# Performance work log

Measured on AMD Instinct MI355X. Metric: run time of the kernel, lower is better.

Reference implementation:

```python
import jax, jax.numpy as jnp
import numpy as np

T, B, D_IN, E, HA, HB, D_OUT = 64, 64, 4096, 128, 128, 128, 4096


def setup_inputs() -> dict:
    key = jax.random.key(0)
    ks = jax.random.split(key, 18)

    def u(k, shape, fan):
        b = 1.0 / np.sqrt(fan)
        return jax.random.uniform(k, shape, jnp.float32, -b, b)

    return {
        "x": jax.random.uniform(ks[0], (T, B, D_IN), jnp.float32),
        "W_emb": u(ks[1], (E, D_IN), D_IN), "b_emb": u(ks[2], (E,), D_IN),
        "W_ih_a": u(ks[3], (3 * HA, E), HA), "W_hh_a": u(ks[4], (3 * HA, HA), HA),
        "b_ih_a": u(ks[5], (3 * HA,), HA), "b_hh_a": u(ks[6], (3 * HA,), HA),
        "W_ih_b": u(ks[7], (3 * HB, E), HB), "W_hh_b": u(ks[8], (3 * HB, HB), HB),
        "b_ih_b": u(ks[9], (3 * HB,), HB), "b_hh_b": u(ks[10], (3 * HB,), HB),
        "w_alpha": u(ks[11], (1, HA), HA), "b_alpha": u(ks[12], (1,), HA),
        "W_beta": u(ks[13], (E, HB), HB), "b_beta": u(ks[14], (E,), HB),
        "W_out": u(ks[15], (D_OUT, E), E), "b_out": u(ks[16], (D_OUT,), E),
    }


def _gru_states(emb, W_ih, W_hh, b_ih, b_hh):
    # For every query position i, run a GRU over the reversed prefix
    # emb[i], emb[i-1], ..., emb[0] from h0 = 0. All T queries are batched.
    # Returns hs[s, i, b, h] = hidden of query i after step s (input emb[i-s]).
    Tlen, Bsz, _ = emb.shape
    H = W_hh.shape[1]
    i_arr = jnp.arange(Tlen)

    def step(h, s):
        idx = jnp.clip(i_arr - s, 0, Tlen - 1)          # (T,) input index per query
        xs = emb[idx]                                    # (T, B, E)
        gi = xs @ W_ih.T + b_ih                          # (T, B, 3H)
        gh = h @ W_hh.T + b_hh
        i_r, i_z, i_n = jnp.split(gi, 3, axis=-1)
        h_r, h_z, h_n = jnp.split(gh, 3, axis=-1)
        r = jax.nn.sigmoid(i_r + h_r)
        z = jax.nn.sigmoid(i_z + h_z)
        n = jnp.tanh(i_n + r * h_n)
        h_new = (1.0 - z) * n + z * h
        return h_new, h_new

    h0 = jnp.zeros((Tlen, Bsz, H), emb.dtype)
    _, hs = jax.lax.scan(step, h0, jnp.arange(Tlen))
    return hs  # (S, T, B, H)


def _retain_forward(x, W_emb, b_emb, W_ih_a, W_hh_a, b_ih_a, b_hh_a,
                    W_ih_b, W_hh_b, b_ih_b, b_hh_b, w_alpha, b_alpha,
                    W_beta, b_beta, W_out, b_out):
    Tlen = x.shape[0]
    emb = x @ W_emb.T + b_emb                            # (T, B, E)

    hs_a = _gru_states(emb, W_ih_a, W_hh_a, b_ih_a, b_hh_a)  # (S, T, B, HA)
    hs_b = _gru_states(emb, W_ih_b, W_hh_b, b_ih_b, b_hh_b)  # (S, T, B, HB)

    i_arr = jnp.arange(Tlen)
    # reverse_h[i, j] = hidden after processing emb[i..j] (reverse order) = hs[i - j, i]
    rev = jnp.clip(i_arr[:, None] - i_arr[None, :], 0, Tlen - 1)  # (T, T)
    rh_a = hs_a[rev, i_arr[:, None]] * 0.5               # (T, T, B, HA)
    rh_b = hs_b[rev, i_arr[:, None]] * 0.5               # (T, T, B, HB)

    mask = (i_arr[None, :] <= i_arr[:, None])            # (T, T): j <= i valid
    logits = jnp.einsum('ijbh,h->ijb', rh_a, w_alpha[0]) + b_alpha[0]
    logits = jnp.where(mask[:, :, None], logits, -1e9)
    alpha = jax.nn.softmax(logits, axis=1)               # softmax over prefix steps j
    alpha = alpha * mask[:, :, None].astype(alpha.dtype)

    beta = jnp.tanh(rh_b @ W_beta.T + b_beta)            # (T, T, B, E)

    # c[i] = mean_{j<=i} alpha[i,j] * beta[i,j] * emb[j]
    c = jnp.einsum('ijb,ijbe->ibe', alpha, beta * emb[None, :, :, :])
    counts = jnp.arange(1, Tlen + 1, dtype=c.dtype)[:, None, None]
    c = c / counts

    return jax.nn.sigmoid(c @ W_out.T + b_out)           # (T, B, D_OUT)


def reference(x, W_emb, b_emb, W_ih_a, W_hh_a, b_ih_a, b_hh_a,
              W_ih_b, W_hh_b, b_ih_b, b_hh_b, w_alpha, b_alpha,
              W_beta, b_beta, W_out, b_out):
    return _retain_forward(x, W_emb, b_emb, W_ih_a, W_hh_a, b_ih_a, b_hh_a,
                           W_ih_b, W_hh_b, b_ih_b, b_hh_b, w_alpha, b_alpha,
                           W_beta, b_beta, W_out, b_out)
```

## Files before the change

kernel.cpp:

```cpp
#include <hip/hip_runtime.h>
#include <hip/hip_bf16.h>


typedef __attribute__((ext_vector_type(8))) short short8;
typedef __attribute__((ext_vector_type(4))) float f32x4;
typedef _Float16 half8 __attribute__((ext_vector_type(8)));

#define MFMA16(a, b, c) __builtin_amdgcn_mfma_f32_16x16x32_bf16((a), (b), (c), 0, 0, 0)

#define LOG2E 1.4426950408889634f
#define TLOG2E 2.8853900817779268f

__device__ __forceinline__ unsigned short f2bf(float f) {
  unsigned int u = __float_as_uint(f);
  u += 0x7fffu + ((u >> 16) & 1u);
  return (unsigned short)(u >> 16);
}
__device__ __forceinline__ unsigned pkbf(float a, float b) {
  __hip_bfloat162 t = __float22bfloat162_rn(float2{a, b});
  return *reinterpret_cast<unsigned*>(&t);
}
__device__ __forceinline__ float ex2(float x) { return __builtin_amdgcn_exp2f(x); }
__device__ __forceinline__ float rcpa(float x) { return __builtin_amdgcn_rcpf(x); }
__device__ __forceinline__ float sigm2(float y) { return rcpa(1.0f + ex2(-y)); }
__device__ __forceinline__ float tanh2(float y) {
  float e = ex2(-fmaxf(y, -126.0f));
  return (1.0f - e) * rcpa(1.0f + e);
}

#define OFF_PART   0u
#define OFF_GI3    16777216u
#define OFF_EMBBF  25165824u
#define OFF_CBF    26214400u
#define OFF_WEMB   27262976u
#define OFF_WOUT   28311552u
#define OFF_WHHA   29360128u
#define OFF_WHHB   29458432u
#define OFF_WIH    29556736u
#define OFF_WBETA  29753344u

__global__ void k_prep(const float* W_emb, const float* W_out,
                       const float* W_hh_a, const float* W_hh_b,
                       const float* W_ih_a, const float* W_ih_b,
                       const float* W_beta,
                       unsigned* wemb, unsigned* wout,
                       unsigned* whha, unsigned* whhb,
                       unsigned* wih, unsigned* wbeta) {
  const unsigned total = 630784u;
  for (unsigned idx = blockIdx.x * 256u + threadIdx.x; idx < total;
       idx += gridDim.x * 256u) {
    unsigned i = idx;
    if (i < 262144u) { float2 v = ((const float2*)W_emb)[i]; wemb[i] = pkbf(v.x, v.y); continue; }
    i -= 262144u;
    if (i < 262144u) { float2 v = ((const float2*)W_out)[i]; wout[i] = pkbf(v.x, v.y); continue; }
    i -= 262144u;
    if (i < 24576u) {
      float2 v = ((const float2*)W_hh_a)[i];
      const float sc = ((i >> 13) == 2u) ? TLOG2E : LOG2E;
      whha[i] = pkbf(sc * v.x, sc * v.y); continue;
    }
    i -= 24576u;
    if (i < 24576u) {
      float2 v = ((const float2*)W_hh_b)[i];
      const float sc = ((i >> 13) == 2u) ? TLOG2E : LOG2E;
      whhb[i] = pkbf(sc * v.x, sc * v.y); continue;
    }
    i -= 24576u;
    if (i < 24576u) {
      float2 v = ((const float2*)W_ih_a)[i];
      const float sc = ((i >> 13) == 2u) ? TLOG2E : LOG2E;
      wih[i] = pkbf(sc * v.x, sc * v.y); continue;
    }
    i -= 24576u;
    if (i < 24576u) {
      float2 v = ((const float2*)W_ih_b)[i];
      const float sc = ((i >> 13) == 2u) ? TLOG2E : LOG2E;
      wih[24576u + i] = pkbf(sc * v.x, sc * v.y); continue;
    }
    i -= 24576u;
    { float2 v = ((const float2*)W_beta)[i]; wbeta[i] = pkbf(LOG2E * v.x, LOG2E * v.y); }
  }
}

__global__ __launch_bounds__(256) void k_emb_gemm(const float* __restrict__ x,
                                                  const unsigned short* __restrict__ wemb,
                                                  float* __restrict__ part) {
  const int mt = blockIdx.x >> 3, kc = blockIdx.x & 7;
  const int w = threadIdx.x >> 6, lane = threadIdx.x & 63, q = lane >> 4, ln = lane & 15;
  const f32x4 zero = {0.f, 0.f, 0.f, 0.f};
  f32x4 acc[2][8];
#pragma unroll
  for (int a = 0; a < 2; ++a)
#pragma unroll
    for (int b = 0; b < 8; ++b) acc[a][b] = zero;

  const float* xA = x + (size_t)(mt * 128 + (2 * w) * 16 + ln) * 4096 + kc * 512 + q * 8;
  const float* xB = xA + (size_t)16 * 4096;

  for (int kk = 0; kk < 16; ++kk) {
    const int ko = kk * 32;
    float4 u0 = *(const float4*)(xA + ko);
    float4 u1 = *(const float4*)(xA + ko + 4);
    float4 v0 = *(const float4*)(xB + ko);
    float4 v1 = *(const float4*)(xB + ko + 4);
    union { short8 v; unsigned u[4]; } a0, a1;
    a0.u[0] = pkbf(u0.x, u0.y); a0.u[1] = pkbf(u0.z, u0.w);
    a0.u[2] = pkbf(u1.x, u1.y); a0.u[3] = pkbf(u1.z, u1.w);
    a1.u[0] = pkbf(v0.x, v0.y); a1.u[1] = pkbf(v0.z, v0.w);
    a1.u[2] = pkbf(v1.x, v1.y); a1.u[3] = pkbf(v1.z, v1.w);
#pragma unroll
    for (int nt = 0; nt < 8; ++nt) {
      short8 b = *(const short8*)(wemb + (size_t)(nt * 16 + ln) * 4096 + kc * 512 + ko + q * 8);
      acc[0][nt] = MFMA16(a0.v, b, acc[0][nt]);
      acc[1][nt] = MFMA16(a1.v, b, acc[1][nt]);
    }
  }
#pragma unroll
  for (int st = 0; st < 2; ++st) {
    const int mbase = mt * 128 + (2 * w + st) * 16 + q * 4;
#pragma unroll
    for (int nt = 0; nt < 8; ++nt)
#pragma unroll
      for (int r = 0; r < 4; ++r)
        part[(size_t)kc * 524288 + (size_t)(mbase + r) * 128 + nt * 16 + ln] = acc[st][nt][r];
  }
}

__global__ void k_emb_reduce(const float* __restrict__ part, const float* __restrict__ b_emb,
                             _Float16* __restrict__ gih, unsigned* __restrict__ embbf) {
  const unsigned pidx = blockIdx.x * 256u + threadIdx.x;
  const unsigned e0 = (pidx * 2u) & 127u;
  const unsigned m = pidx >> 6;
  float2 s = ((const float2*)b_emb)[e0 >> 1];
#pragma unroll
  for (int kc = 0; kc < 8; ++kc) {
    float2 v = ((const float2*)(part + (size_t)kc * 524288u))[pidx];
    s.x += v.x; s.y += v.y;
  }
  gih[(size_t)m * 1024u + e0 * 8u + 6u] = (_Float16)s.x;
  gih[(size_t)m * 1024u + (e0 + 1u) * 8u + 6u] = (_Float16)s.y;
  embbf[pidx] = pkbf(s.x, s.y);
}

__global__ __launch_bounds__(256) void k_gi_gemm(const unsigned short* __restrict__ embbf,
                                                 const unsigned short* __restrict__ wih,
                                                 const float* __restrict__ b_ih_a,
                                                 const float* __restrict__ b_ih_b,
                                                 const float* __restrict__ b_hh_a,
                                                 const float* __restrict__ b_hh_b,
                                                 _Float16* __restrict__ gih) {
  const int mt = blockIdx.x / 6, nt6 = blockIdx.x % 6, nbase = nt6 * 128;
  const int w = threadIdx.x >> 6, lane = threadIdx.x & 63, q = lane >> 4, ln = lane & 15;
  const f32x4 zero = {0.f, 0.f, 0.f, 0.f};
  f32x4 acc[2][8];
#pragma unroll
  for (int a = 0; a < 2; ++a)
#pragma unroll
    for (int b = 0; b < 8; ++b) acc[a][b] = zero;

#pragma unroll
  for (int kk = 0; kk < 4; ++kk) {
    const int ko = kk * 32 + q * 8;
    short8 a0 = *(const short8*)(embbf + (size_t)(mt * 128 + (2 * w) * 16 + ln) * 128 + ko);
    short8 a1 = *(const short8*)(embbf + (size_t)(mt * 128 + (2 * w + 1) * 16 + ln) * 128 + ko);
#pragma unroll
    for (int nt = 0; nt < 8; ++nt) {
      short8 b = *(const short8*)(wih + (size_t)(nbase + nt * 16 + ln) * 128 + ko);
      acc[0][nt] = MFMA16(a0, b, acc[0][nt]);
      acc[1][nt] = MFMA16(a1, b, acc[1][nt]);
    }
  }
#pragma unroll
  for (int nt = 0; nt < 8; ++nt) {
    const int g = nbase + nt * 16 + ln;
    const int gg = g >> 7, kout = g & 127;
    float bias;
    if (g < 384) bias = b_ih_a[g] + ((gg < 2) ? b_hh_a[g] : 0.0f);
    else {
      const int g2 = g - 384;
      bias = b_ih_b[g2] + ((gg < 5) ? b_hh_b[g2] : 0.0f);
    }
    bias *= (gg == 2 || gg == 5) ? TLOG2E : LOG2E;
#pragma unroll
    for (int st = 0; st < 2; ++st) {
      const int mbase = mt * 128 + (2 * w + st) * 16 + q * 4;
#pragma unroll
      for (int r = 0; r < 4; ++r)
        gih[(size_t)(mbase + r) * 1024 + kout * 8 + gg] = (_Float16)(acc[st][nt][r] + bias);
    }
  }
}

__global__ __launch_bounds__(512) __attribute__((amdgpu_waves_per_eu(2, 2)))
void k_recur(const _Float16* __restrict__ gih,
             const unsigned short* __restrict__ whha, const unsigned short* __restrict__ whhb,
             const unsigned short* __restrict__ wbeta,
             const float* __restrict__ b_hh_a, const float* __restrict__ b_hh_b,
             const float* __restrict__ b_beta, const float* __restrict__ b_alpha,
             const float* __restrict__ w_alpha,
             unsigned short* __restrict__ cbf) {
  const int tid = threadIdx.x, w = tid >> 6, lane = tid & 63, q = lane >> 4, ln = lane & 15;
  const int p = blockIdx.x >> 3, btile = blockIdx.x & 7;
  const int i1 = p, i2 = 63 - p;
  const int kout = w * 16 + ln;

  __shared__ unsigned short hA[2][16 * 136], hB[2][16 * 136];

  for (int idx = tid; idx < 16 * 136; idx += 512) { hA[0][idx] = 0; hB[0][idx] = 0; }

  const int iq = (q < 2) ? i1 : i2;
  const _Float16* gp[4];
#pragma unroll
  for (int r = 0; r < 4; ++r) {
    const int b = btile * 8 + (q & 1) * 4 + r;
    gp[r] = gih + (size_t)(iq * 64 + b) * 1024 + kout * 8;
  }

  short8 fra[3][4], frb[3][4];
#pragma unroll
  for (int g = 0; g < 3; ++g) {
    const unsigned short* ba = whha + (size_t)(g * 128 + kout) * 128;
    const unsigned short* bb = whhb + (size_t)(g * 128 + kout) * 128;
#pragma unroll
    for (int kc = 0; kc < 4; ++kc) {
      fra[g][kc] = *(const short8*)(ba + kc * 32 + q * 8);
      frb[g][kc] = *(const short8*)(bb + kc * 32 + q * 8);
    }
  }
#pragma unroll
  for (int g = 0; g < 3; ++g)
#pragma unroll
    for (int kc = 0; kc < 4; ++kc) {
      asm volatile("" : "+a"(fra[g][kc]));
      asm volatile("" : "+a"(frb[g][kc]));
    }

  short8 fbe[4];
#pragma unroll
  for (int kc = 0; kc < 4; ++kc) {
    fbe[kc] = *(const short8*)(wbeta + (size_t)(w * 16 + ln) * 128 + kc * 32 + q * 8);
    asm volatile("" : "+a"(fbe[kc]));
  }

  short8 fal[4];
#pragma unroll
  for (int kc = 0; kc < 4; ++kc) {
    float4 w0 = *(const float4*)(w_alpha + kc * 32 + q * 8);
    float4 w1 = *(const float4*)(w_alpha + kc * 32 + q * 8 + 4);
    union { short8 v; unsigned u[4]; } t;
    t.u[0] = pkbf(0.5f * LOG2E * w0.x, 0.5f * LOG2E * w0.y);
    t.u[1] = pkbf(0.5f * LOG2E * w0.z, 0.5f * LOG2E * w0.w);
    t.u[2] = pkbf(0.5f * LOG2E * w1.x, 0.5f * LOG2E * w1.y);
    t.u[3] = pkbf(0.5f * LOG2E * w1.z, 0.5f * LOG2E * w1.w);
    const short8 z8 = {0, 0, 0, 0, 0, 0, 0, 0};
    fal[kc] = (ln == 0) ? t.v : z8;
    asm volatile("" : "+a"(fal[kc]));
  }

  const float bhnA = TLOG2E * b_hh_a[256 + kout];
  const float bhnB = TLOG2E * b_hh_b[256 + kout];
  const float bbet = TLOG2E * b_beta[kout];
  const float bal = LOG2E * b_alpha[0];

  float hRA[4], hRB[4], cac[4], lreg[4], embp[4];
#pragma unroll
  for (int r = 0; r < 4; ++r) { hRA[r] = 0.f; hRB[r] = 0.f; cac[r] = 0.f; lreg[r] = 0.f; embp[r] = 0.f; }

  const f32x4 zero = {0.f, 0.f, 0.f, 0.f};
  int jj = iq;
  half8 ngv[4];
#pragma unroll
  for (int r = 0; r < 4; ++r) ngv[r] = *(const half8*)gp[r];

  __syncthreads();

  for (int s = 0; s <= i2; ++s) {
    const int rb = s & 1, wb = rb ^ 1;

    half8 gv[4];
#pragma unroll
    for (int r = 0; r < 4; ++r) gv[r] = ngv[r];

    short8 haf[4], hbf[4];
#pragma unroll
    for (int kc = 0; kc < 4; ++kc) {
      haf[kc] = *(const short8*)(hA[rb] + ln * 136 + kc * 32 + q * 8);
      hbf[kc] = *(const short8*)(hB[rb] + ln * 136 + kc * 32 + q * 8);
    }

    f32x4 accA[3] = {zero, zero, zero}, accB[3] = {zero, zero, zero};
    f32x4 accV = zero, accL = zero;
#pragma unroll
    for (int kc = 0; kc < 4; ++kc) {
#pragma unroll
      for (int g = 0; g < 3; ++g) {
        accA[g] = MFMA16(haf[kc], fra[g][kc], accA[g]);
        accB[g] = MFMA16(hbf[kc], frb[g][kc], accB[g]);
      }
      accV = MFMA16(hbf[kc], fbe[kc], accV);
      accL = MFMA16(haf[kc], fal[kc], accL);
    }

    const bool act = ((unsigned)(s - 1) <= (unsigned)iq);
#pragma unroll
    for (int r = 0; r < 4; ++r) {
      const float logit =
          __int_as_float(__builtin_amdgcn_ds_swizzle(__float_as_int(accL[r]), 16)) + bal;
      const float pp = act ? ex2(logit) : 0.0f;
      lreg[r] += pp;
      const float beta = tanh2(accV[r] + bbet);
      cac[r] += pp * beta * embp[r];
    }

#pragma unroll
    for (int r = 0; r < 4; ++r) {
      const int rowoff = (q * 4 + r) * 136 + kout;
      const float rrA = sigm2((float)gv[r][0] + accA[0][r]);
      const float zzA = sigm2((float)gv[r][1] + accA[1][r]);
      const float nnA = tanh2((float)gv[r][2] + rrA * (accA[2][r] + bhnA));
      const float hnA = fmaf(zzA, hRA[r] - nnA, nnA);
      hRA[r] = hnA;
      hA[wb][rowoff] = f2bf(hnA);

      const float rrB = sigm2((float)gv[r][3] + accB[0][r]);
      const float zzB = sigm2((float)gv[r][4] + accB[1][r]);
      const float nnB = tanh2((float)gv[r][5] + rrB * (accB[2][r] + bhnB));
      const float hnB = fmaf(zzB, hRB[r] - nnB, nnB);
      hRB[r] = hnB;
      hB[wb][rowoff] = f2bf(hnB);

      embp[r] = (float)gv[r][6];
    }

    if (jj > 0) {
      --jj;
#pragma unroll
      for (int r = 0; r < 4; ++r) gp[r] -= 65536;
    }
#pragma unroll
    for (int r = 0; r < 4; ++r) ngv[r] = *(const half8*)gp[r];

    asm volatile("s_waitcnt lgkmcnt(0)\n\ts_barrier" ::: "memory");
  }

  {
    const int rb2 = (i2 + 1) & 1;
    short8 haf[4], hbf[4];
#pragma unroll
    for (int kc = 0; kc < 4; ++kc) {
      haf[kc] = *(const short8*)(hA[rb2] + ln * 136 + kc * 32 + q * 8);
      hbf[kc] = *(const short8*)(hB[rb2] + ln * 136 + kc * 32 + q * 8);
    }
    f32x4 accV = zero, accL = zero;
#pragma unroll
    for (int kc = 0; kc < 4; ++kc) {
      accV = MFMA16(hbf[kc], fbe[kc], accV);
      accL = MFMA16(haf[kc], fal[kc], accL);
    }
    const bool act = (iq == i2);
#pragma unroll
    for (int r = 0; r < 4; ++r) {
      const float logit =
          __int_as_float(__builtin_amdgcn_ds_swizzle(__float_as_int(accL[r]), 16)) + bal;
      const float pp = act ? ex2(logit) : 0.0f;
      lreg[r] += pp;
      const float beta = tanh2(accV[r] + bbet);
      cac[r] += pp * beta * embp[r];
    }
  }

#pragma unroll
  for (int r = 0; r < 4; ++r) {
    const int b = btile * 8 + (q & 1) * 4 + r;
    const float val = cac[r] * rcpa(lreg[r] * (float)(iq + 1));
    cbf[(size_t)(iq * 64 + b) * 128 + kout] = f2bf(val);
  }
}

__global__ __launch_bounds__(256) void k_out_gemm(const unsigned short* __restrict__ cbf,
                                                  const unsigned short* __restrict__ wout,
                                                  const float* __restrict__ b_out,
                                                  float* __restrict__ out) {
  const int mt = blockIdx.x >> 5, nt32 = blockIdx.x & 31, nbase = nt32 * 128;
  const int w = threadIdx.x >> 6, lane = threadIdx.x & 63, q = lane >> 4, ln = lane & 15;
  const f32x4 zero = {0.f, 0.f, 0.f, 0.f};
  f32x4 acc[2][8];
#pragma unroll
  for (int a = 0; a < 2; ++a)
#pragma unroll
    for (int b = 0; b < 8; ++b) acc[a][b] = zero;

#pragma unroll
  for (int kk = 0; kk < 4; ++kk) {
    const int ko = kk * 32 + q * 8;
    short8 a0 = *(const short8*)(cbf + (size_t)(mt * 128 + (2 * w) * 16 + ln) * 128 + ko);
    short8 a1 = *(const short8*)(cbf + (size_t)(mt * 128 + (2 * w + 1) * 16 + ln) * 128 + ko);
#pragma unroll
    for (int nt = 0; nt < 8; ++nt) {
      short8 b = *(const short8*)(wout + (size_t)(nbase + nt * 16 + ln) * 128 + ko);
      acc[0][nt] = MFMA16(a0, b, acc[0][nt]);
      acc[1][nt] = MFMA16(a1, b, acc[1][nt]);
    }
  }
#pragma unroll
  for (int nt = 0; nt < 8; ++nt) {
    const int n = nbase + nt * 16 + ln;
    const float bo = b_out[n];
#pragma unroll
    for (int st = 0; st < 2; ++st) {
      const int mbase = mt * 128 + (2 * w + st) * 16 + q * 4;
#pragma unroll
      for (int r = 0; r < 4; ++r)
        out[(size_t)(mbase + r) * 4096 + n] =
            rcpa(1.0f + ex2(-LOG2E * (acc[st][nt][r] + bo)));
    }
  }
}

extern "C" void kernel_launch(void* const* d_in, const int* in_sizes, int n_in,
                              void* d_out, int out_size, void* d_ws, size_t ws_size,
                              hipStream_t stream) {
  const float* x      = (const float*)d_in[0];
  const float* W_emb  = (const float*)d_in[1];
  const float* b_emb  = (const float*)d_in[2];
  const float* W_ih_a = (const float*)d_in[3];
  const float* W_hh_a = (const float*)d_in[4];
  const float* b_ih_a = (const float*)d_in[5];
  const float* b_hh_a = (const float*)d_in[6];
  const float* W_ih_b = (const float*)d_in[7];
  const float* W_hh_b = (const float*)d_in[8];
  const float* b_ih_b = (const float*)d_in[9];
  const float* b_hh_b = (const float*)d_in[10];
  const float* w_alpha = (const float*)d_in[11];
  const float* b_alpha = (const float*)d_in[12];
  const float* W_beta = (const float*)d_in[13];
  const float* b_beta = (const float*)d_in[14];
  const float* W_out  = (const float*)d_in[15];
  const float* b_out  = (const float*)d_in[16];
  float* out = (float*)d_out;

  char* ws = (char*)d_ws;
  float*          part   = (float*)(ws + OFF_PART);
  _Float16*       gih    = (_Float16*)(ws + OFF_GI3);
  unsigned*       embbf  = (unsigned*)(ws + OFF_EMBBF);
  unsigned short* cbf    = (unsigned short*)(ws + OFF_CBF);
  unsigned*       wemb   = (unsigned*)(ws + OFF_WEMB);
  unsigned*       wout   = (unsigned*)(ws + OFF_WOUT);
  unsigned*       whha   = (unsigned*)(ws + OFF_WHHA);
  unsigned*       whhb   = (unsigned*)(ws + OFF_WHHB);
  unsigned*       wih    = (unsigned*)(ws + OFF_WIH);
  unsigned*       wbeta  = (unsigned*)(ws + OFF_WBETA);

  k_prep<<<1024, 256, 0, stream>>>(W_emb, W_out, W_hh_a, W_hh_b, W_ih_a, W_ih_b,
                                   W_beta, wemb, wout, whha, whhb, wih, wbeta);
  k_emb_gemm<<<256, 256, 0, stream>>>(x, (const unsigned short*)wemb, part);
  k_emb_reduce<<<1024, 256, 0, stream>>>(part, b_emb, gih, embbf);
  k_gi_gemm<<<192, 256, 0, stream>>>((const unsigned short*)embbf, (const unsigned short*)wih,
                                     b_ih_a, b_ih_b, b_hh_a, b_hh_b, gih);
  k_recur<<<256, 512, 0, stream>>>(gih, (const unsigned short*)whha,
                                   (const unsigned short*)whhb, (const unsigned short*)wbeta,
                                   b_hh_a, b_hh_b, b_beta, b_alpha, w_alpha, cbf);
  k_out_gemm<<<1024, 256, 0, stream>>>(cbf, (const unsigned short*)wout, b_out, out);
}
```

Before: 343.8 us.

## Retile emb and out GEMMs and fuse GRU gate math into fewer transcendentals

Result: no change. 344.8 us (+0.3%).

```diff
diff --git a/kernel.cpp b/kernel.cpp
--- a/kernel.cpp
+++ b/kernel.cpp
@@ -11,18 +11,12 @@
 #define LOG2E 1.4426950408889634f
 #define TLOG2E 2.8853900817779268f
 
-__device__ __forceinline__ unsigned short f2bf(float f) {
-  unsigned int u = __float_as_uint(f);
-  u += 0x7fffu + ((u >> 16) & 1u);
-  return (unsigned short)(u >> 16);
-}
 __device__ __forceinline__ unsigned pkbf(float a, float b) {
   __hip_bfloat162 t = __float22bfloat162_rn(float2{a, b});
   return *reinterpret_cast<unsigned*>(&t);
 }
 __device__ __forceinline__ float ex2(float x) { return __builtin_amdgcn_exp2f(x); }
 __device__ __forceinline__ float rcpa(float x) { return __builtin_amdgcn_rcpf(x); }
-__device__ __forceinline__ float sigm2(float y) { return rcpa(1.0f + ex2(-y)); }
 __device__ __forceinline__ float tanh2(float y) {
   float e = ex2(-fmaxf(y, -126.0f));
   return (1.0f - e) * rcpa(1.0f + e);
@@ -88,42 +82,31 @@
   const int mt = blockIdx.x >> 3, kc = blockIdx.x & 7;
   const int w = threadIdx.x >> 6, lane = threadIdx.x & 63, q = lane >> 4, ln = lane & 15;
   const f32x4 zero = {0.f, 0.f, 0.f, 0.f};
-  f32x4 acc[2][8];
-#pragma unroll
-  for (int a = 0; a < 2; ++a)
-#pragma unroll
-    for (int b = 0; b < 8; ++b) acc[a][b] = zero;
-
-  const float* xA = x + (size_t)(mt * 128 + (2 * w) * 16 + ln) * 4096 + kc * 512 + q * 8;
-  const float* xB = xA + (size_t)16 * 4096;
+  f32x4 acc[8];
+#pragma unroll
+  for (int b = 0; b < 8; ++b) acc[b] = zero;
+
+  const float* xA = x + (size_t)(mt * 64 + w * 16 + ln) * 4096 + kc * 512 + q * 8;
 
   for (int kk = 0; kk < 16; ++kk) {
     const int ko = kk * 32;
     float4 u0 = *(const float4*)(xA + ko);
     float4 u1 = *(const float4*)(xA + ko + 4);
-    float4 v0 = *(const float4*)(xB + ko);
-    float4 v1 = *(const float4*)(xB + ko + 4);
-    union { short8 v; unsigned u[4]; } a0, a1;
+    union { short8 v; unsigned u[4]; } a0;
     a0.u[0] = pkbf(u0.x, u0.y); a0.u[1] = pkbf(u0.z, u0.w);
     a0.u[2] = pkbf(u1.x, u1.y); a0.u[3] = pkbf(u1.z, u1.w);
-    a1.u[0] = pkbf(v0.x, v0.y); a1.u[1] = pkbf(v0.z, v0.w);
-    a1.u[2] = pkbf(v1.x, v1.y); a1.u[3] = pkbf(v1.z, v1.w);
 #pragma unroll
     for (int nt = 0; nt < 8; ++nt) {
       short8 b = *(const short8*)(wemb + (size_t)(nt * 16 + ln) * 4096 + kc * 512 + ko + q * 8);
-      acc[0][nt] = MFMA16(a0.v, b, acc[0][nt]);
-      acc[1][nt] = MFMA16(a1.v, b, acc[1][nt]);
-    }
-  }
-#pragma unroll
-  for (int st = 0; st < 2; ++st) {
-    const int mbase = mt * 128 + (2 * w + st) * 16 + q * 4;
-#pragma unroll
-    for (int nt = 0; nt < 8; ++nt)
-#pragma unroll
-      for (int r = 0; r < 4; ++r)
-        part[(size_t)kc * 524288 + (size_t)(mbase + r) * 128 + nt * 16 + ln] = acc[st][nt][r];
-  }
+      acc[nt] = MFMA16(a0.v, b, acc[nt]);
+    }
+  }
+  const int mbase = mt * 64 + w * 16 + q * 4;
+#pragma unroll
+  for (int nt = 0; nt < 8; ++nt)
+#pragma unroll
+    for (int r = 0; r < 4; ++r)
+      part[(size_t)kc * 524288 + (size_t)(mbase + r) * 128 + nt * 16 + ln] = acc[nt][r];
 }
 
 __global__ void k_emb_reduce(const float* __restrict__ part, const float* __restrict__ b_emb,
@@ -315,19 +298,28 @@
 #pragma unroll
     for (int r = 0; r < 4; ++r) {
       const int rowoff = (q * 4 + r) * 136 + kout;
-      const float rrA = sigm2((float)gv[r][0] + accA[0][r]);
-      const float zzA = sigm2((float)gv[r][1] + accA[1][r]);
-      const float nnA = tanh2((float)gv[r][2] + rrA * (accA[2][r] + bhnA));
-      const float hnA = fmaf(zzA, hRA[r] - nnA, nnA);
+
+      const float erA = ex2(-((float)gv[r][0] + accA[0][r]));
+      const float rA = rcpa(1.0f + erA);
+      const float tA = (float)gv[r][2] + rA * (accA[2][r] + bhnA);
+      const float enA = ex2(-fmaxf(tA, -62.0f));
+      const float ezA = ex2(-fmaxf((float)gv[r][1] + accA[1][r], -62.0f));
+      const float apnA = 1.0f + enA, apzA = 1.0f + ezA;
+      const float numA = fmaf(hRA[r], apnA, ezA * (1.0f - enA));
+      const float hnA = numA * rcpa(apnA * apzA);
       hRA[r] = hnA;
-      hA[wb][rowoff] = f2bf(hnA);
-
-      const float rrB = sigm2((float)gv[r][3] + accB[0][r]);
-      const float zzB = sigm2((float)gv[r][4] + accB[1][r]);
-      const float nnB = tanh2((float)gv[r][5] + rrB * (accB[2][r] + bhnB));
-      const float hnB = fmaf(zzB, hRB[r] - nnB, nnB);
+      hA[wb][rowoff] = (unsigned short)pkbf(hnA, hnA);
+
+      const float erB = ex2(-((float)gv[r][3] + accB[0][r]));
+      const float rB = rcpa(1.0f + erB);
+      const float tB = (float)gv[r][5] + rB * (accB[2][r] + bhnB);
+      const float enB = ex2(-fmaxf(tB, -62.0f));
+      const float ezB = ex2(-fmaxf((float)gv[r][4] + accB[1][r], -62.0f));
+      const float apnB = 1.0f + enB, apzB = 1.0f + ezB;
+      const float numB = fmaf(hRB[r], apnB, ezB * (1.0f - enB));
+      const float hnB = numB * rcpa(apnB * apzB);
       hRB[r] = hnB;
-      hB[wb][rowoff] = f2bf(hnB);
+      hB[wb][rowoff] = (unsigned short)pkbf(hnB, hnB);
 
       embp[r] = (float)gv[r][6];
     }
@@ -373,7 +365,7 @@
   for (int r = 0; r < 4; ++r) {
     const int b = btile * 8 + (q & 1) * 4 + r;
     const float val = cac[r] * rcpa(lreg[r] * (float)(iq + 1));
-    cbf[(size_t)(iq * 64 + b) * 128 + kout] = f2bf(val);
+    cbf[(size_t)(iq * 64 + b) * 128 + kout] = (unsigned short)pkbf(val, val);
   }
 }
 
@@ -381,38 +373,36 @@
                                                   const unsigned short* __restrict__ wout,
                                                   const float* __restrict__ b_out,
                                                   float* __restrict__ out) {
-  const int mt = blockIdx.x >> 5, nt32 = blockIdx.x & 31, nbase = nt32 * 128;
+  const int mt = blockIdx.x >> 7, ntb = blockIdx.x & 127, nbase = ntb * 32;
   const int w = threadIdx.x >> 6, lane = threadIdx.x & 63, q = lane >> 4, ln = lane & 15;
   const f32x4 zero = {0.f, 0.f, 0.f, 0.f};
-  f32x4 acc[2][8];
-#pragma unroll
-  for (int a = 0; a < 2; ++a)
-#pragma unroll
-    for (int b = 0; b < 8; ++b) acc[a][b] = zero;
+  f32x4 acc[2][2] = {{zero, zero}, {zero, zero}};
 
 #pragma unroll
   for (int kk = 0; kk < 4; ++kk) {
     const int ko = kk * 32 + q * 8;
-    short8 a0 = *(const short8*)(cbf + (size_t)(mt * 128 + (2 * w) * 16 + ln) * 128 + ko);
-    short8 a1 = *(const short8*)(cbf + (size_t)(mt * 128 + (2 * w + 1) * 16 + ln) * 128 + ko);
-#pragma unroll
-    for (int nt = 0; nt < 8; ++nt) {
-      short8 b = *(const short8*)(wout + (size_t)(nbase + nt * 16 + ln) * 128 + ko);
-      acc[0][nt] = MFMA16(a0, b, acc[0][nt]);
-      acc[1][nt] = MFMA16(a1, b, acc[1][nt]);
-    }
-  }
-#pragma unroll
-  for (int nt = 0; nt < 8; ++nt) {
-    const int n = nbase + nt * 16 + ln;
-    const float bo = b_out[n];
-#pragma unroll
-    for (int st = 0; st < 2; ++st) {
-      const int mbase = mt * 128 + (2 * w + st) * 16 + q * 4;
-#pragma unroll
-      for (int r = 0; r < 4; ++r)
-        out[(size_t)(mbase + r) * 4096 + n] =
-            rcpa(1.0f + ex2(-LOG2E * (acc[st][nt][r] + bo)));
+    short8 a0 = *(const short8*)(wout + (size_t)(nbase + ln) * 128 + ko);
+    short8 a1 = *(const short8*)(wout + (size_t)(nbase + 16 + ln) * 128 + ko);
+    short8 b0 = *(const short8*)(cbf + (size_t)(mt * 128 + (w * 2 + 0) * 16 + ln) * 128 + ko);
+    short8 b1 = *(const short8*)(cbf + (size_t)(mt * 128 + (w * 2 + 1) * 16 + ln) * 128 + ko);
+    acc[0][0] = MFMA16(a0, b0, acc[0][0]);
+    acc[0][1] = MFMA16(a0, b1, acc[0][1]);
+    acc[1][0] = MFMA16(a1, b0, acc[1][0]);
+    acc[1][1] = MFMA16(a1, b1, acc[1][1]);
+  }
+#pragma unroll
+  for (int st = 0; st < 2; ++st) {
+    const int n0 = nbase + st * 16 + q * 4;
+    const float4 bo = *(const float4*)(b_out + n0);
+#pragma unroll
+    for (int j = 0; j < 2; ++j) {
+      const int m = mt * 128 + (w * 2 + j) * 16 + ln;
+      float4 o;
+      o.x = rcpa(1.0f + ex2(-LOG2E * (acc[st][j][0] + bo.x)));
+      o.y = rcpa(1.0f + ex2(-LOG2E * (acc[st][j][1] + bo.y)));
+      o.z = rcpa(1.0f + ex2(-LOG2E * (acc[st][j][2] + bo.z)));
+      o.w = rcpa(1.0f + ex2(-LOG2E * (acc[st][j][3] + bo.w)));
+      *(float4*)(out + (size_t)m * 4096 + n0) = o;
     }
   }
 }
@@ -453,12 +443,12 @@
 
   k_prep<<<1024, 256, 0, stream>>>(W_emb, W_out, W_hh_a, W_hh_b, W_ih_a, W_ih_b,
                                    W_beta, wemb, wout, whha, whhb, wih, wbeta);
-  k_emb_gemm<<<256, 256, 0, stream>>>(x, (const unsigned short*)wemb, part);
+  k_emb_gemm<<<512, 256, 0, stream>>>(x, (const unsigned short*)wemb, part);
   k_emb_reduce<<<1024, 256, 0, stream>>>(part, b_emb, gih, embbf);
   k_gi_gemm<<<192, 256, 0, stream>>>((const unsigned short*)embbf, (const unsigned short*)wih,
                                      b_ih_a, b_ih_b, b_hh_a, b_hh_b, gih);
   k_recur<<<256, 512, 0, stream>>>(gih, (const unsigned short*)whha,
                                    (const unsigned short*)whhb, (const unsigned short*)wbeta,
                                    b_hh_a, b_hh_b, b_beta, b_alpha, w_alpha, cbf);
-  k_out_gemm<<<1024, 256, 0, stream>>>(cbf, (const unsigned short*)wout, b_out, out);
-}
+  k_out_gemm<<<4096, 256, 0, stream>>>(cbf, (const unsigned short*)wout, b_out, out);
+}
```
